# Kernel tuning notes

Measured on AMD Instinct MI355X. Metric: run time of the kernel, lower is better.

## Reference

```python
import jax, jax.numpy as jnp
import numpy as np

WB = 8   # weight bit width (signed int8, power-of-two scale)
AB = 8   # activation bit width (uint8, power-of-two scale)
BB = 8   # bias bit width

# (name, c_in, c_out, kernel) for every QuantConv2d in order
_CFG = [("1", 3, 32, 3), ("2", 32, 16, 3), ("31", 16, 16, 1), ("32", 16, 32, 3),
        ("33", 32, 32, 1), ("34", 32, 64, 3), ("41", 64, 32, 1), ("42", 32, 64, 3),
        ("43", 64, 32, 1), ("44", 32, 64, 3), ("45", 64, 32, 1), ("46", 32, 64, 3)]
_POOL_AFTER = {"1", "2", "34"}  # MaxPool2d(2,2) follows these blocks


def _ste_round(x):
    # straight-through rounding (Brevitas-style fake quant)
    return x + jax.lax.stop_gradient(jnp.round(x) - x)


def _p2_scale(maxv, levels):
    # power-of-two (fixed point) per-tensor scale covering maxv with `levels` steps
    maxv = jnp.maximum(jax.lax.stop_gradient(maxv), 1e-8)
    return 2.0 ** jnp.ceil(jnp.log2(maxv / levels))


def quant_int(x, bw):
    # signed symmetric fixed-point fake quant (Int8WeightPerTensorFixedPoint style)
    n = 2.0 ** (bw - 1) - 1.0
    s = _p2_scale(jnp.max(jnp.abs(x)), n)
    return jnp.clip(_ste_round(x / s), -n - 1.0, n) * s


def quant_uint(x, bw):
    # unsigned fixed-point fake quant (Uint8ActPerTensorFixedPoint style)
    n = 2.0 ** bw - 1.0
    s = _p2_scale(jnp.max(x), n)
    return jnp.clip(_ste_round(x / s), 0.0, n) * s


def _conv(x, w, pad):
    return jax.lax.conv_general_dilated(
        x, w, window_strides=(1, 1), padding=[(pad, pad), (pad, pad)],
        dimension_numbers=("NCHW", "OIHW", "NCHW"))


def _maxpool2(x):
    return jax.lax.reduce_window(x, -jnp.inf, jax.lax.max,
                                 (1, 1, 2, 2), (1, 1, 2, 2), "VALID")


def _forward(x, p):
    # QuantIdentity on input (uint8 fixed point)
    x = quant_uint(x, AB)
    for n, ci, co, k in _CFG:
        pad = (k - 1) // 2
        y = _conv(x, quant_int(p["w" + n], WB), pad)               # quantized conv, no bias
        # BatchNorm2dToQuantScaleBias: per-channel affine with quantized scale/bias
        y = (y * quant_int(p["sg" + n], WB)[None, :, None, None]
             + quant_int(p["sb" + n], BB)[None, :, None, None])
        x = quant_uint(jax.nn.relu(y), AB)                          # QuantReLU
        if n in _POOL_AFTER:
            x = _maxpool2(x)
    # TruncAvgPool2d(28,28) over the remaining 28x28 map + RoundTo8bit requant
    x = quant_uint(jnp.mean(x, axis=(2, 3)), 8)                     # [B, 64]
    h = x @ quant_int(p["fw1"], WB).T + quant_int(p["fb1"], BB)     # linear51
    h = quant_uint(jax.nn.relu(h), AB)                              # relu5
    return h @ quant_int(p["fw2"], WB).T + quant_int(p["fb2"], BB)  # linear52


def setup_inputs() -> dict:
    key = jax.random.key(0)
    ks = iter(jax.random.split(key, 64))
    inp = {"x": jax.random.uniform(next(ks), (16, 3, 224, 224), jnp.float32)}
    for n, ci, co, k in _CFG:
        inp["w" + n] = jax.random.normal(next(ks), (co, ci, k, k), jnp.float32) * 0.1
        inp["sg" + n] = jax.random.uniform(next(ks), (co,), jnp.float32, 0.5, 1.5)
        inp["sb" + n] = jax.random.normal(next(ks), (co,), jnp.float32) * 0.1
    inp["fw1"] = jax.random.normal(next(ks), (16, 64), jnp.float32) * 0.1
    inp["fb1"] = jax.random.normal(next(ks), (16,), jnp.float32) * 0.1
    inp["fw2"] = jax.random.normal(next(ks), (10, 16), jnp.float32) * 0.1
    inp["fb2"] = jax.random.normal(next(ks), (10,), jnp.float32) * 0.1
    return inp


def reference(x, w1, sg1, sb1, w2, sg2, sb2, w31, sg31, sb31, w32, sg32, sb32,
              w33, sg33, sb33, w34, sg34, sb34, w41, sg41, sb41, w42, sg42, sb42,
              w43, sg43, sb43, w44, sg44, sb44, w45, sg45, sb45, w46, sg46, sb46,
              fw1, fb1, fw2, fb2):
    p = dict(locals())
    x = p.pop("x")
    return _forward(x, p)
```

## Files before the change

kernel.cpp:

```cpp
#include <hip/hip_runtime.h>
#include <math.h>

#define NL 12

typedef short v8s __attribute__((ext_vector_type(8)));
typedef float v4f __attribute__((ext_vector_type(4)));

struct PrepArgs {
  const float* in[40];
  void* out[40];
  int n[40];
  int mode[40];
  int tc[40];
  int ci[40], kk[40], kp[40], co[40];
};

__device__ inline float p2_scale_f(float maxv, float levels) {
  float r = __fdiv_rn(fmaxf(maxv, 1e-8f), levels);
  unsigned b = __float_as_uint(r);
  unsigned e = (b >> 23) & 0xffu;
  e += (b & 0x7fffffu) ? 1u : 0u;
  return __uint_as_float(e << 23);
}

__device__ inline float p2_inv(float s) {
  return __uint_as_float((254u << 23) - __float_as_uint(s));
}

__device__ inline float block_reduce_max256(float v) {
  __shared__ float sm[4];
  #pragma unroll
  for (int off = 32; off; off >>= 1) v = fmaxf(v, __shfl_down(v, off));
  if ((threadIdx.x & 63) == 0) sm[threadIdx.x >> 6] = v;
  __syncthreads();
  if (threadIdx.x == 0) v = fmaxf(fmaxf(sm[0], sm[1]), fmaxf(sm[2], sm[3]));
  return v;
}

__device__ inline void slot_max_update(float* slot, float v) {
  volatile unsigned int* su = (volatile unsigned int*)slot;
  unsigned int bits = __float_as_uint(v);
  if (bits > *su) atomicMax((unsigned int*)slot, bits);
}

__device__ inline short ibf16(float v) {
  return (short)(__float_as_uint(v) >> 16);
}

__global__ void prep_kernel(PrepArgs a, float* wslot,
                            const float* __restrict__ x, int nx, float* slot0) {
  if (blockIdx.x >= 40) {
    const float4* xv = (const float4*)x;
    const int nv = nx >> 2;
    float m0 = 0.f, m1 = 0.f, m2 = 0.f, m3 = 0.f;
    for (int i = (blockIdx.x - 40) * 256 + threadIdx.x; i < nv;
         i += (gridDim.x - 40) * 256) {
      float4 v = xv[i];
      m0 = fmaxf(m0, v.x); m1 = fmaxf(m1, v.y);
      m2 = fmaxf(m2, v.z); m3 = fmaxf(m3, v.w);
    }
    float m = fmaxf(fmaxf(m0, m1), fmaxf(m2, m3));
    float bm = block_reduce_max256(m);
    if (threadIdx.x == 0) slot_max_update(slot0, bm);
    return;
  }
  __shared__ float ssc;
  const int t = blockIdx.x;
  const float* in = a.in[t];
  const int n = a.n[t], mode = a.mode[t];
  float m = 0.f;
  if (mode == 2) {
    const float4* in4 = (const float4*)in;
    const int n4 = n >> 2;
    for (int i = threadIdx.x; i < n4; i += 256) {
      float4 v = in4[i];
      m = fmaxf(m, fmaxf(fmaxf(fabsf(v.x), fabsf(v.y)),
                         fmaxf(fabsf(v.z), fabsf(v.w))));
    }
  } else {
    for (int i = threadIdx.x; i < n; i += 256) m = fmaxf(m, fabsf(in[i]));
  }
  float bm = block_reduce_max256(m);
  if (threadIdx.x == 0) {
    ssc = p2_scale_f(bm, 127.0f);
    if (mode == 2) wslot[t] = ssc;
  }
  __syncthreads();
  const float s = ssc;
  if (mode == 2) {
    ushort* o = (ushort*)a.out[t];
    const int CI = a.ci[t], KK = a.kk[t], KP = a.kp[t], CO = a.co[t];
    const int KT = CI * KK;
    for (int i = threadIdx.x; i < CO * KP; i += 256) {
      int co = i / KP, k = i % KP;
      ushort v = 0;
      if (k < KT) {
        int khkw = k / CI, ci = k % CI;
        float q = rintf(__fdiv_rn(in[(co * CI + ci) * KK + khkw], s));
        q = fminf(fmaxf(q, -128.f), 127.f);
        v = (ushort)(__float_as_uint(q) >> 16);
      }
      o[i] = v;
    }
  } else {
    float* o = (float*)a.out[t];
    const int tc = a.tc[t];
    const int nw = (mode == 1) ? n / tc : 1;
    for (int i = threadIdx.x; i < n; i += 256) {
      float q = rintf(__fdiv_rn(in[i], s));
      q = fminf(fmaxf(q, -128.f), 127.f);
      float v = __fmul_rn(q, s);
      if (mode == 1) o[(i % nw) * tc + i / nw] = v;
      else o[i] = v;
    }
  }
}


template <int CI, int H, int CO, bool K3, bool POOL>
__global__ __launch_bounds__(256)
void conv_mfma(const float* __restrict__ in, const short* __restrict__ wt,
               const float* __restrict__ sg, const float* __restrict__ sb,
               float* __restrict__ out, const float* __restrict__ slot_in,
               const float* __restrict__ wslotp, float* slot_out) {
  constexpr int W = H;
  constexpr int KT = (K3 ? 9 : 1) * CI;
  constexpr int SLABS = (KT + 31) / 32;
  constexpr int KP = SLABS * 32;
  constexpr int COT = CO / 16;
  constexpr int HO = POOL ? H / 2 : H;
  constexpr int WO = POOL ? W / 2 : W;

  const int lane = threadIdx.x & 63, widx = threadIdx.x >> 6;
  const int quad = lane >> 4, col = lane & 15;
  const float s_in = p2_scale_f(slot_in[0], 255.0f);
  const float inv = p2_inv(s_in);
  const float S = __fmul_rn(s_in, wslotp[0]);
  const int wv = blockIdx.x * 4 + widx;

  int n, h, w, ph = 0, pw = 0;
  if constexpr (POOL) {
    constexpr int PB = (HO / 2) * (WO / 2);
    n = wv / PB; int r = wv % PB;
    ph = r / (WO / 2); pw = r % (WO / 2);
    h = 4 * ph + (col >> 2); w = 4 * pw + (col & 3);
  } else {
    int p = wv * 16 + col;
    n = p / (H * W); int r = p % (H * W);
    h = r / W; w = r % W;
  }
  const float* ibase = in + (size_t)n * H * W * CI;

  v4f acc[COT];
  #pragma unroll
  for (int c = 0; c < COT; c++) acc[c] = (v4f){0.f, 0.f, 0.f, 0.f};

  #pragma unroll
  for (int slab = 0; slab < SLABS; slab++) {
    const int kbase = slab * 32 + quad * 8;
    v8s a;
    if constexpr (K3) {
      int khkw = kbase / CI; khkw = min(khkw, 8);
      const int cib = kbase % CI;
      const int kh = khkw / 3, kw = khkw - kh * 3;
      const int hh = h + kh - 1, ww = w + kw - 1;
      const bool valid = (hh >= 0) && (hh < H) && (ww >= 0) && (ww < W) && (kbase < KT);
      const int hc = min(max(hh, 0), H - 1), wc = min(max(ww, 0), W - 1);
      const float* ap = ibase + (size_t)(hc * W + wc) * CI + cib;
      float4 f0 = ((const float4*)ap)[0];
      float4 f1 = ((const float4*)ap)[1];
      float ff[8] = {f0.x, f0.y, f0.z, f0.w, f1.x, f1.y, f1.z, f1.w};
      #pragma unroll
      for (int j = 0; j < 8; j++) {
        float q = rintf(__fmul_rn(ff[j], inv));
        a[j] = valid ? ibf16(q) : (short)0;
      }
    } else {
      const int cib = kbase % CI;
      const float* ap = ibase + (size_t)(h * W + w) * CI + cib;
      float4 f0 = ((const float4*)ap)[0];
      float4 f1 = ((const float4*)ap)[1];
      float ff[8] = {f0.x, f0.y, f0.z, f0.w, f1.x, f1.y, f1.z, f1.w};
      #pragma unroll
      for (int j = 0; j < 8; j++) a[j] = ibf16(rintf(__fmul_rn(ff[j], inv)));
    }
    #pragma unroll
    for (int c = 0; c < COT; c++) {
      v8s b = *(const v8s*)(wt + (size_t)(c * 16 + col) * KP + kbase);
      acc[c] = __builtin_amdgcn_mfma_f32_16x16x32_bf16(a, b, acc[c], 0, 0, 0);
    }
  }

  float zmax = 0.f;
  #pragma unroll
  for (int c = 0; c < COT; c++) {
    const int cog = c * 16 + col;
    const float g = sg[cog], bb = sb[cog];
    float z[4];
    #pragma unroll
    for (int r2 = 0; r2 < 4; r2++) {
      float t = __fmul_rn(acc[c][r2], S);
      z[r2] = fmaxf(__fadd_rn(__fmul_rn(t, g), bb), 0.f);
    }
    if constexpr (POOL) {
      float h0 = fmaxf(z[0], z[1]), h1 = fmaxf(z[2], z[3]);
      float o0 = fmaxf(h0, __shfl_xor(h0, 16));
      float o1 = fmaxf(h1, __shfl_xor(h1, 16));
      zmax = fmaxf(zmax, fmaxf(o0, o1));
      if (!(quad & 1)) {
        int oh = 2 * ph + (quad >> 1), ow = 2 * pw;
        float* op = out + ((size_t)((n * HO + oh) * WO + ow)) * CO + cog;
        op[0] = o0; op[CO] = o1;
      }
    } else {
      const int pbase = wv * 16 + quad * 4;
      #pragma unroll
      for (int r2 = 0; r2 < 4; r2++) {
        out[(size_t)(pbase + r2) * CO + cog] = z[r2];
        zmax = fmaxf(zmax, z[r2]);
      }
    }
  }
  float bm = block_reduce_max256(zmax);
  if (threadIdx.x == 0) slot_max_update(slot_out, bm);
}

__global__ __launch_bounds__(256)
void conv1_mfma(const float* __restrict__ x, const short* __restrict__ wt,
                const float* __restrict__ sg, const float* __restrict__ sb,
                float* __restrict__ out, const float* __restrict__ slot_in,
                const float* __restrict__ wslotp, float* slot_out) {
  const int lane = threadIdx.x & 63, widx = threadIdx.x >> 6;
  const int quad = lane >> 4, col = lane & 15;
  const float s_in = p2_scale_f(slot_in[0], 255.0f);
  const float inv = p2_inv(s_in);
  const float S = __fmul_rn(s_in, wslotp[0]);
  const int wv = blockIdx.x * 4 + widx;
  const int n = wv / 3136, r = wv % 3136;
  const int ph = r / 56, pw = r % 56;
  const int h = 4 * ph + (col >> 2), w = 4 * pw + (col & 3);

  v8s a;
  #pragma unroll
  for (int j = 0; j < 8; j++) {
    int k = quad * 8 + j;
    int kc = min(k, 26);
    int khkw = kc / 3, ci = kc - khkw * 3;
    int kh = khkw / 3, kw = khkw - kh * 3;
    int hh = h + kh - 1, ww = w + kw - 1;
    bool valid = (k < 27) && (hh >= 0) && (hh < 224) && (ww >= 0) && (ww < 224);
    int hc = min(max(hh, 0), 223), wc = min(max(ww, 0), 223);
    float v = x[((n * 3 + ci) * 224 + hc) * 224 + wc];
    float q = rintf(__fmul_rn(v, inv));
    a[j] = valid ? ibf16(q) : (short)0;
  }
  v4f acc[2];
  acc[0] = (v4f){0.f, 0.f, 0.f, 0.f};
  acc[1] = acc[0];
  #pragma unroll
  for (int c = 0; c < 2; c++) {
    v8s b = *(const v8s*)(wt + (size_t)(c * 16 + col) * 32 + quad * 8);
    acc[c] = __builtin_amdgcn_mfma_f32_16x16x32_bf16(a, b, acc[c], 0, 0, 0);
  }
  float zmax = 0.f;
  #pragma unroll
  for (int c = 0; c < 2; c++) {
    const int cog = c * 16 + col;
    const float g = sg[cog], bb = sb[cog];
    float z[4];
    #pragma unroll
    for (int r2 = 0; r2 < 4; r2++) {
      float t = __fmul_rn(acc[c][r2], S);
      z[r2] = fmaxf(__fadd_rn(__fmul_rn(t, g), bb), 0.f);
    }
    float h0 = fmaxf(z[0], z[1]), h1 = fmaxf(z[2], z[3]);
    float o0 = fmaxf(h0, __shfl_xor(h0, 16));
    float o1 = fmaxf(h1, __shfl_xor(h1, 16));
    zmax = fmaxf(zmax, fmaxf(o0, o1));
    if (!(quad & 1)) {
      int oh = 2 * ph + (quad >> 1), ow = 2 * pw;
      float* op = out + ((size_t)((n * 112 + oh) * 112 + ow)) * 32 + cog;
      op[0] = o0; op[32] = o1;
    }
  }
  float bm = block_reduce_max256(zmax);
  if (threadIdx.x == 0) slot_max_update(slot_out, bm);
}

__global__ void avgpool_kernel(const float* __restrict__ in, float* __restrict__ out,
                               const float* __restrict__ slot_in, float* slot_out) {
  __shared__ float red[256];
  const float s = p2_scale_f(slot_in[0], 255.0f);
  const float inv = p2_inv(s);
  const int nn = blockIdx.x, co = threadIdx.x & 63, part = threadIdx.x >> 6;
  const float* p = in + (size_t)nn * 784 * 64;
  float sum = 0.f;
  for (int i = part * 196; i < part * 196 + 196; i++)
    sum += __fmul_rn(rintf(__fmul_rn(p[i * 64 + co], inv)), s);
  red[threadIdx.x] = sum;
  __syncthreads();
  if (threadIdx.x < 64) {
    float tot = (red[co] + red[64 + co]) + (red[128 + co] + red[192 + co]);
    float m = __fdiv_rn(tot, 784.0f);
    out[nn * 64 + co] = m;
    slot_max_update(slot_out, m);
  }
}

__global__ void tail_kernel(const float* __restrict__ pooled,
                            const float* __restrict__ fw1, const float* __restrict__ fb1,
                            const float* __restrict__ fw2, const float* __restrict__ fb2,
                            const float* __restrict__ slot_in, float* __restrict__ out) {
  __shared__ float xq[1024];
  __shared__ float hq[256];
  __shared__ float s2s;
  const int t = threadIdx.x;
  const float s = p2_scale_f(slot_in[0], 255.0f);
  const float inv = p2_inv(s);
  for (int i = t; i < 1024; i += 256)
    xq[i] = __fmul_rn(rintf(__fmul_rn(pooled[i], inv)), s);
  __syncthreads();
  const int n = t >> 4, j = t & 15;
  float acc = 0.f;
  #pragma unroll 8
  for (int k = 0; k < 64; k++) acc += xq[n * 64 + k] * fw1[k * 16 + j];
  float z = fmaxf(__fadd_rn(acc, fb1[j]), 0.f);
  float bm = block_reduce_max256(z);
  if (t == 0) s2s = p2_scale_f(bm, 255.0f);
  __syncthreads();
  const float s2 = s2s, inv2 = p2_inv(s2);
  hq[t] = __fmul_rn(rintf(__fmul_rn(z, inv2)), s2);
  __syncthreads();
  if (t < 160) {
    const int n2 = t / 10, j2 = t % 10;
    float a2 = 0.f;
    #pragma unroll
    for (int k = 0; k < 16; k++) a2 += hq[n2 * 16 + k] * fw2[k * 10 + j2];
    out[t] = __fadd_rn(a2, fb2[j2]);
  }
}

extern "C" void kernel_launch(void* const* d_in, const int* in_sizes, int n_in,
                              void* d_out, int out_size, void* d_ws, size_t ws_size,
                              hipStream_t stream) {
  static const int h_ci[NL] = {3, 32, 16, 16, 32, 32, 64, 32, 64, 32, 64, 32};
  static const int h_co[NL] = {32, 16, 16, 32, 32, 64, 32, 64, 32, 64, 32, 64};
  static const int h_kk[NL] = {9, 9, 1, 9, 1, 9, 1, 9, 1, 9, 1, 9};
  static const int h_kp[NL] = {32, 288, 32, 160, 32, 288, 64, 288, 64, 288, 64, 288};

  float* ws = (float*)d_ws;
  float* slots = ws;
  float* wslot = ws + 16;
  size_t off = 32;

  short* wq[NL];
  for (int l = 0; l < NL; l++) {
    wq[l] = (short*)(ws + off);
    off += (size_t)(h_co[l] * h_kp[l] + 1) / 2;
  }
  float* sgq[NL]; float* sbq[NL];
  for (int l = 0; l < NL; l++) { sgq[l] = ws + off; off += 64; }
  for (int l = 0; l < NL; l++) { sbq[l] = ws + off; off += 64; }
  float* fw1q = ws + off; off += 1024;
  float* fb1q = ws + off; off += 16;
  float* fw2q = ws + off; off += 160;
  float* fb2q = ws + off; off += 16;
  float* A = ws + off; off += 6422528;
  float* B = ws + off; off += 1605632;
  float* P = ws + off; off += 1024;

  PrepArgs pa;
  for (int l = 0; l < NL; l++) {
    pa.in[l] = (const float*)d_in[1 + 3 * l]; pa.out[l] = (void*)wq[l];
    pa.n[l] = h_co[l] * h_ci[l] * h_kk[l];
    pa.mode[l] = 2; pa.tc[l] = 0;
    pa.ci[l] = h_ci[l]; pa.kk[l] = h_kk[l]; pa.kp[l] = h_kp[l]; pa.co[l] = h_co[l];
    pa.in[12 + l] = (const float*)d_in[2 + 3 * l]; pa.out[12 + l] = (void*)sgq[l];
    pa.n[12 + l] = h_co[l]; pa.mode[12 + l] = 0; pa.tc[12 + l] = 0;
    pa.ci[12 + l] = pa.kk[12 + l] = pa.kp[12 + l] = pa.co[12 + l] = 0;
    pa.in[24 + l] = (const float*)d_in[3 + 3 * l]; pa.out[24 + l] = (void*)sbq[l];
    pa.n[24 + l] = h_co[l]; pa.mode[24 + l] = 0; pa.tc[24 + l] = 0;
    pa.ci[24 + l] = pa.kk[24 + l] = pa.kp[24 + l] = pa.co[24 + l] = 0;
  }
  pa.in[36] = (const float*)d_in[37]; pa.out[36] = (void*)fw1q;
  pa.n[36] = 1024; pa.mode[36] = 1; pa.tc[36] = 16;
  pa.ci[36] = pa.kk[36] = pa.kp[36] = pa.co[36] = 0;
  pa.in[37] = (const float*)d_in[38]; pa.out[37] = (void*)fb1q;
  pa.n[37] = 16; pa.mode[37] = 0; pa.tc[37] = 0;
  pa.ci[37] = pa.kk[37] = pa.kp[37] = pa.co[37] = 0;
  pa.in[38] = (const float*)d_in[39]; pa.out[38] = (void*)fw2q;
  pa.n[38] = 160; pa.mode[38] = 1; pa.tc[38] = 10;
  pa.ci[38] = pa.kk[38] = pa.kp[38] = pa.co[38] = 0;
  pa.in[39] = (const float*)d_in[40]; pa.out[39] = (void*)fb2q;
  pa.n[39] = 10; pa.mode[39] = 0; pa.tc[39] = 0;
  pa.ci[39] = pa.kk[39] = pa.kp[39] = pa.co[39] = 0;

  const float* x = (const float*)d_in[0];
  const int nx = 16 * 3 * 224 * 224;

  hipMemsetAsync(slots, 0, 16 * sizeof(float), stream);
  prep_kernel<<<40 + 294, 256, 0, stream>>>(pa, wslot, x, nx, slots + 0);

  conv1_mfma<<<12544, 256, 0, stream>>>(x, wq[0], sgq[0], sbq[0], A,
                                        slots + 0, wslot + 0, slots + 1);
  conv_mfma<32, 112, 16, true, true><<<3136, 256, 0, stream>>>(
      A, wq[1], sgq[1], sbq[1], B, slots + 1, wslot + 1, slots + 2);
  conv_mfma<16, 56, 16, false, false><<<784, 256, 0, stream>>>(
      B, wq[2], sgq[2], sbq[2], A, slots + 2, wslot + 2, slots + 3);
  conv_mfma<16, 56, 32, true, false><<<784, 256, 0, stream>>>(
      A, wq[3], sgq[3], sbq[3], B, slots + 3, wslot + 3, slots + 4);
  conv_mfma<32, 56, 32, false, false><<<784, 256, 0, stream>>>(
      B, wq[4], sgq[4], sbq[4], A, slots + 4, wslot + 4, slots + 5);
  conv_mfma<32, 56, 64, true, true><<<784, 256, 0, stream>>>(
      A, wq[5], sgq[5], sbq[5], B, slots + 5, wslot + 5, slots + 6);
  conv_mfma<64, 28, 32, false, false><<<196, 256, 0, stream>>>(
      B, wq[6], sgq[6], sbq[6], A, slots + 6, wslot + 6, slots + 7);
  conv_mfma<32, 28, 64, true, false><<<196, 256, 0, stream>>>(
      A, wq[7], sgq[7], sbq[7], B, slots + 7, wslot + 7, slots + 8);
  conv_mfma<64, 28, 32, false, false><<<196, 256, 0, stream>>>(
      B, wq[8], sgq[8], sbq[8], A, slots + 8, wslot + 8, slots + 9);
  conv_mfma<32, 28, 64, true, false><<<196, 256, 0, stream>>>(
      A, wq[9], sgq[9], sbq[9], B, slots + 9, wslot + 9, slots + 10);
  conv_mfma<64, 28, 32, false, false><<<196, 256, 0, stream>>>(
      B, wq[10], sgq[10], sbq[10], A, slots + 10, wslot + 10, slots + 11);
  conv_mfma<32, 28, 64, true, false><<<196, 256, 0, stream>>>(
      A, wq[11], sgq[11], sbq[11], B, slots + 11, wslot + 11, slots + 12);

  avgpool_kernel<<<16, 256, 0, stream>>>(B, P, slots + 12, slots + 13);
  tail_kernel<<<1, 256, 0, stream>>>(P, fw1q, fb1q, fw2q, fb2q, slots + 13,
                                     (float*)d_out);
}
```

Measured before the change: 367.3 us.

## Split output channels across waves, hoist activation loads, widen avgpool block

Adds a CSPLIT template parameter so each wave computes only a slice of the output channels. This doubles the grid for the later conv layers so more waves are in flight on the small 28x28 and 56x56 layers. All activation loads for every K slab are now issued before any MFMA to raise memory-level parallelism, and conv1 likewise batches its gathers. The avgpool kernel goes to 1024 threads with a 16-way partial reduction. In exchange, each input activation is loaded and quantized once per channel slice, and more registers are held per thread.

```diff
diff --git a/kernel.cpp b/kernel.cpp
--- a/kernel.cpp
+++ b/kernel.cpp
@@ -117,7 +117,7 @@
 }
 
 
-template <int CI, int H, int CO, bool K3, bool POOL>
+template <int CI, int H, int CO, bool K3, bool POOL, int CSPLIT>
 __global__ __launch_bounds__(256)
 void conv_mfma(const float* __restrict__ in, const short* __restrict__ wt,
                const float* __restrict__ sg, const float* __restrict__ sb,
@@ -127,7 +127,7 @@
   constexpr int KT = (K3 ? 9 : 1) * CI;
   constexpr int SLABS = (KT + 31) / 32;
   constexpr int KP = SLABS * 32;
-  constexpr int COT = CO / 16;
+  constexpr int COT = CO / (16 * CSPLIT);
   constexpr int HO = POOL ? H / 2 : H;
   constexpr int WO = POOL ? W / 2 : W;
 
@@ -137,56 +137,61 @@
   const float inv = p2_inv(s_in);
   const float S = __fmul_rn(s_in, wslotp[0]);
   const int wv = blockIdx.x * 4 + widx;
+  const int mt = wv / CSPLIT, ct = wv % CSPLIT;
 
   int n, h, w, ph = 0, pw = 0;
   if constexpr (POOL) {
     constexpr int PB = (HO / 2) * (WO / 2);
-    n = wv / PB; int r = wv % PB;
+    n = mt / PB; int r = mt % PB;
     ph = r / (WO / 2); pw = r % (WO / 2);
     h = 4 * ph + (col >> 2); w = 4 * pw + (col & 3);
   } else {
-    int p = wv * 16 + col;
+    int p = mt * 16 + col;
     n = p / (H * W); int r = p % (H * W);
     h = r / W; w = r % W;
   }
   const float* ibase = in + (size_t)n * H * W * CI;
 
-  v4f acc[COT];
-  #pragma unroll
-  for (int c = 0; c < COT; c++) acc[c] = (v4f){0.f, 0.f, 0.f, 0.f};
-
+  float4 fa[SLABS], fb[SLABS];
+  bool vm[SLABS];
   #pragma unroll
   for (int slab = 0; slab < SLABS; slab++) {
     const int kbase = slab * 32 + quad * 8;
-    v8s a;
+    const float* ap;
     if constexpr (K3) {
-      int khkw = kbase / CI; khkw = min(khkw, 8);
+      const int khkw = min(kbase / CI, 8);
       const int cib = kbase % CI;
       const int kh = khkw / 3, kw = khkw - kh * 3;
       const int hh = h + kh - 1, ww = w + kw - 1;
-      const bool valid = (hh >= 0) && (hh < H) && (ww >= 0) && (ww < W) && (kbase < KT);
+      vm[slab] = (hh >= 0) && (hh < H) && (ww >= 0) && (ww < W);
       const int hc = min(max(hh, 0), H - 1), wc = min(max(ww, 0), W - 1);
-      const float* ap = ibase + (size_t)(hc * W + wc) * CI + cib;
-      float4 f0 = ((const float4*)ap)[0];
-      float4 f1 = ((const float4*)ap)[1];
-      float ff[8] = {f0.x, f0.y, f0.z, f0.w, f1.x, f1.y, f1.z, f1.w};
-      #pragma unroll
-      for (int j = 0; j < 8; j++) {
-        float q = rintf(__fmul_rn(ff[j], inv));
-        a[j] = valid ? ibf16(q) : (short)0;
-      }
+      ap = ibase + (size_t)(hc * W + wc) * CI + cib;
     } else {
-      const int cib = kbase % CI;
-      const float* ap = ibase + (size_t)(h * W + w) * CI + cib;
-      float4 f0 = ((const float4*)ap)[0];
-      float4 f1 = ((const float4*)ap)[1];
-      float ff[8] = {f0.x, f0.y, f0.z, f0.w, f1.x, f1.y, f1.z, f1.w};
-      #pragma unroll
-      for (int j = 0; j < 8; j++) a[j] = ibf16(rintf(__fmul_rn(ff[j], inv)));
+      vm[slab] = true;
+      ap = ibase + (size_t)(h * W + w) * CI + (kbase % CI);
+    }
+    fa[slab] = ((const float4*)ap)[0];
+    fb[slab] = ((const float4*)ap)[1];
+  }
+
+  v4f acc[COT];
+  #pragma unroll
+  for (int c = 0; c < COT; c++) acc[c] = (v4f){0.f, 0.f, 0.f, 0.f};
+
+  #pragma unroll
+  for (int slab = 0; slab < SLABS; slab++) {
+    const int kbase = slab * 32 + quad * 8;
+    float ff[8] = {fa[slab].x, fa[slab].y, fa[slab].z, fa[slab].w,
+                   fb[slab].x, fb[slab].y, fb[slab].z, fb[slab].w};
+    v8s a;
+    #pragma unroll
+    for (int j = 0; j < 8; j++) {
+      float q = rintf(__fmul_rn(ff[j], inv));
+      a[j] = vm[slab] ? ibf16(q) : (short)0;
     }
     #pragma unroll
     for (int c = 0; c < COT; c++) {
-      v8s b = *(const v8s*)(wt + (size_t)(c * 16 + col) * KP + kbase);
+      v8s b = *(const v8s*)(wt + (size_t)((ct * COT + c) * 16 + col) * KP + kbase);
       acc[c] = __builtin_amdgcn_mfma_f32_16x16x32_bf16(a, b, acc[c], 0, 0, 0);
     }
   }
@@ -194,7 +199,7 @@
   float zmax = 0.f;
   #pragma unroll
   for (int c = 0; c < COT; c++) {
-    const int cog = c * 16 + col;
+    const int cog = (ct * COT + c) * 16 + col;
     const float g = sg[cog], bb = sb[cog];
     float z[4];
     #pragma unroll
@@ -213,7 +218,7 @@
         op[0] = o0; op[CO] = o1;
       }
     } else {
-      const int pbase = wv * 16 + quad * 4;
+      const int pbase = mt * 16 + quad * 4;
       #pragma unroll
       for (int r2 = 0; r2 < 4; r2++) {
         out[(size_t)(pbase + r2) * CO + cog] = z[r2];
@@ -240,7 +245,8 @@
   const int ph = r / 56, pw = r % 56;
   const int h = 4 * ph + (col >> 2), w = 4 * pw + (col & 3);
 
-  v8s a;
+  float fv[8];
+  bool vm[8];
   #pragma unroll
   for (int j = 0; j < 8; j++) {
     int k = quad * 8 + j;
@@ -248,11 +254,15 @@
     int khkw = kc / 3, ci = kc - khkw * 3;
     int kh = khkw / 3, kw = khkw - kh * 3;
     int hh = h + kh - 1, ww = w + kw - 1;
-    bool valid = (k < 27) && (hh >= 0) && (hh < 224) && (ww >= 0) && (ww < 224);
+    vm[j] = (hh >= 0) && (hh < 224) && (ww >= 0) && (ww < 224);
     int hc = min(max(hh, 0), 223), wc = min(max(ww, 0), 223);
-    float v = x[((n * 3 + ci) * 224 + hc) * 224 + wc];
-    float q = rintf(__fmul_rn(v, inv));
-    a[j] = valid ? ibf16(q) : (short)0;
+    fv[j] = x[((n * 3 + ci) * 224 + hc) * 224 + wc];
+  }
+  v8s a;
+  #pragma unroll
+  for (int j = 0; j < 8; j++) {
+    float q = rintf(__fmul_rn(fv[j], inv));
+    a[j] = vm[j] ? ibf16(q) : (short)0;
   }
   v4f acc[2];
   acc[0] = (v4f){0.f, 0.f, 0.f, 0.f};
@@ -289,18 +299,20 @@
 
 __global__ void avgpool_kernel(const float* __restrict__ in, float* __restrict__ out,
                                const float* __restrict__ slot_in, float* slot_out) {
-  __shared__ float red[256];
+  __shared__ float red[1024];
   const float s = p2_scale_f(slot_in[0], 255.0f);
   const float inv = p2_inv(s);
   const int nn = blockIdx.x, co = threadIdx.x & 63, part = threadIdx.x >> 6;
   const float* p = in + (size_t)nn * 784 * 64;
   float sum = 0.f;
-  for (int i = part * 196; i < part * 196 + 196; i++)
+  for (int i = part * 49; i < part * 49 + 49; i++)
     sum += __fmul_rn(rintf(__fmul_rn(p[i * 64 + co], inv)), s);
   red[threadIdx.x] = sum;
   __syncthreads();
   if (threadIdx.x < 64) {
-    float tot = (red[co] + red[64 + co]) + (red[128 + co] + red[192 + co]);
+    float tot = 0.f;
+    #pragma unroll
+    for (int k2 = 0; k2 < 16; k2++) tot += red[k2 * 64 + co];
     float m = __fdiv_rn(tot, 784.0f);
     out[nn * 64 + co] = m;
     slot_max_update(slot_out, m);
@@ -403,30 +415,30 @@
 
   conv1_mfma<<<12544, 256, 0, stream>>>(x, wq[0], sgq[0], sbq[0], A,
                                         slots + 0, wslot + 0, slots + 1);
-  conv_mfma<32, 112, 16, true, true><<<3136, 256, 0, stream>>>(
+  conv_mfma<32, 112, 16, true, true, 1><<<3136, 256, 0, stream>>>(
       A, wq[1], sgq[1], sbq[1], B, slots + 1, wslot + 1, slots + 2);
-  conv_mfma<16, 56, 16, false, false><<<784, 256, 0, stream>>>(
+  conv_mfma<16, 56, 16, false, false, 1><<<784, 256, 0, stream>>>(
       B, wq[2], sgq[2], sbq[2], A, slots + 2, wslot + 2, slots + 3);
-  conv_mfma<16, 56, 32, true, false><<<784, 256, 0, stream>>>(
+  conv_mfma<16, 56, 32, true, false, 2><<<1568, 256, 0, stream>>>(
       A, wq[3], sgq[3], sbq[3], B, slots + 3, wslot + 3, slots + 4);
-  conv_mfma<32, 56, 32, false, false><<<784, 256, 0, stream>>>(
+  conv_mfma<32, 56, 32, false, false, 2><<<1568, 256, 0, stream>>>(
       B, wq[4], sgq[4], sbq[4], A, slots + 4, wslot + 4, slots + 5);
-  conv_mfma<32, 56, 64, true, true><<<784, 256, 0, stream>>>(
+  conv_mfma<32, 56, 64, true, true, 2><<<1568, 256, 0, stream>>>(
       A, wq[5], sgq[5], sbq[5], B, slots + 5, wslot + 5, slots + 6);
-  conv_mfma<64, 28, 32, false, false><<<196, 256, 0, stream>>>(
+  conv_mfma<64, 28, 32, false, false, 2><<<392, 256, 0, stream>>>(
       B, wq[6], sgq[6], sbq[6], A, slots + 6, wslot + 6, slots + 7);
-  conv_mfma<32, 28, 64, true, false><<<196, 256, 0, stream>>>(
+  conv_mfma<32, 28, 64, true, false, 2><<<392, 256, 0, stream>>>(
       A, wq[7], sgq[7], sbq[7], B, slots + 7, wslot + 7, slots + 8);
-  conv_mfma<64, 28, 32, false, false><<<196, 256, 0, stream>>>(
+  conv_mfma<64, 28, 32, false, false, 2><<<392, 256, 0, stream>>>(
       B, wq[8], sgq[8], sbq[8], A, slots + 8, wslot + 8, slots + 9);
-  conv_mfma<32, 28, 64, true, false><<<196, 256, 0, stream>>>(
+  conv_mfma<32, 28, 64, true, false, 2><<<392, 256, 0, stream>>>(
       A, wq[9], sgq[9], sbq[9], B, slots + 9, wslot + 9, slots + 10);
-  conv_mfma<64, 28, 32, false, false><<<196, 256, 0, stream>>>(
+  conv_mfma<64, 28, 32, false, false, 2><<<392, 256, 0, stream>>>(
       B, wq[10], sgq[10], sbq[10], A, slots + 10, wslot + 10, slots + 11);
-  conv_mfma<32, 28, 64, true, false><<<196, 256, 0, stream>>>(
+  conv_mfma<32, 28, 64, true, false, 2><<<392, 256, 0, stream>>>(
       A, wq[11], sgq[11], sbq[11], B, slots + 11, wslot + 11, slots + 12);
 
-  avgpool_kernel<<<16, 256, 0, stream>>>(B, P, slots + 12, slots + 13);
+  avgpool_kernel<<<16, 1024, 0, stream>>>(B, P, slots + 12, slots + 13);
   tail_kernel<<<1, 256, 0, stream>>>(P, fw1q, fb1q, fw2q, fb2q, slots + 13,
                                      (float*)d_out);
 }
```

New measurement: 383.2 us. +4.3%, slower.
